# Performance work log

Hardware: AMD Instinct MI355X
Metric: run time of the kernel (lower is better)

## Reference

```python
import jax, jax.numpy as jnp
import numpy as np
from jax import lax

SEQ, B, I, H, O = 512, 64, 512, 1024, 512


def _linear_params(key, out_f, in_f):
    kw, kb = jax.random.split(key)
    bound = 1.0 / np.sqrt(in_f)
    W = jax.random.uniform(kw, (out_f, in_f), jnp.float32, -bound, bound)
    b = jax.random.uniform(kb, (out_f,), jnp.float32, -bound, bound)
    return W, b


def setup_inputs() -> dict:
    key = jax.random.key(0)
    ks = jax.random.split(key, 8)
    x = jax.random.normal(ks[0], (SEQ, B, I), jnp.float32)
    Wxz, bxz = _linear_params(ks[1], H, I)
    Whz, bhz = _linear_params(ks[2], H, H)
    Wxr, bxr = _linear_params(ks[3], H, I)
    Whr, bhr = _linear_params(ks[4], H, H)
    Wxh, bxh = _linear_params(ks[5], H, I)
    Whh, bhh = _linear_params(ks[6], H, H)
    Why, bhy = _linear_params(ks[7], O, H)
    return {"x": x, "Wxz": Wxz, "bxz": bxz, "Whz": Whz, "bhz": bhz,
            "Wxr": Wxr, "bxr": bxr, "Whr": Whr, "bhr": bhr,
            "Wxh": Wxh, "bxh": bxh, "Whh": Whh, "bhh": bhh,
            "Why": Why, "bhy": bhy}


def reference(x, Wxz, bxz, Whz, bhz, Wxr, bxr, Whr, bhr, Wxh, bxh, Whh, bhh, Why, bhy):
    # Precompute all input-side projections in batched GEMMs: [S,B,H]
    xz = jnp.einsum('sbi,hi->sbh', x, Wxz) + bxz
    xr = jnp.einsum('sbi,hi->sbh', x, Wxr) + bxr
    xh = jnp.einsum('sbi,hi->sbh', x, Wxh) + bxh

    def step(h, inp):
        xz_t, xr_t, xh_t = inp
        z = jax.nn.sigmoid(xz_t + h @ Whz.T + bhz)
        r = jax.nn.sigmoid(xr_t + h @ Whr.T + bhr)
        h_cand = jnp.tanh(xh_t + r * (h @ Whh.T + bhh))
        h_new = (1.0 - z) * h + z * h_cand
        return h_new, h_new

    h0 = jnp.zeros((x.shape[1], Whz.shape[0]), x.dtype)
    _, hs = lax.scan(step, h0, (xz, xr, xh))  # hs: [S,B,H]
    out = jnp.einsum('sbh,oh->sbo', hs, Why) + bhy  # [S,B,O]
    return out
```

## Files before the change

### kernel.cpp

```cpp
#include <hip/hip_runtime.h>
#include <hip/hip_bf16.h>

#define SEQL 512
#define BATCH 64
#define INF 512
#define HID 1024
#define OUTF 512
#define SB (SEQL*BATCH)
#define BH (BATCH*HID)

typedef __attribute__((ext_vector_type(8))) __bf16 bf16x8;
typedef __attribute__((ext_vector_type(4))) float f32x4;

__device__ inline bf16x8 ld_bf8(const void* p) { return *reinterpret_cast<const bf16x8*>(p); }
__device__ inline unsigned short f2bf(float f) { __bf16 b = (__bf16)f; return __builtin_bit_cast(unsigned short, b); }

__device__ inline void st_u64c(void* p, unsigned long long v) {
    __hip_atomic_store((unsigned long long*)p, v, __ATOMIC_RELAXED, __HIP_MEMORY_SCOPE_AGENT);
}

__global__ void cvt_f32_bf16(const float* __restrict__ src, unsigned short* __restrict__ dst, int n) {
    int i = (blockIdx.x * blockDim.x + threadIdx.x) * 4;
    if (i < n) {
        float4 v = *reinterpret_cast<const float4*>(src + i);
        ushort4 o = make_ushort4(f2bf(v.x), f2bf(v.y), f2bf(v.z), f2bf(v.w));
        *reinterpret_cast<ushort4*>(dst + i) = o;
    }
}

__global__ void make_bias2(const float* bxz, const float* bhz, const float* bxr,
                           const float* bhr, float* bias2) {
    int i = blockIdx.x * blockDim.x + threadIdx.x;
    if (i < HID) bias2[i] = bxz[i] + bhz[i];
    else if (i < 2*HID) bias2[i] = bxr[i-HID] + bhr[i-HID];
}

__global__ void fail_sentinel(float* o) { o[0] = 1e9f; }

__global__ __launch_bounds__(256, 2) void gemm_nt_f32(
        const unsigned short* __restrict__ A, int lda,
        const unsigned short* __restrict__ Bw, int ldb,
        const float* __restrict__ bias,
        float* __restrict__ Cf, int N, int K) {
    __shared__ __align__(16) char lds[32768];
    const int tid = threadIdx.x;
    const int ntn = N >> 7;
    const int bm = blockIdx.x / ntn, bn = blockIdx.x % ntn;
    const int rowbase = bm << 7, colbase = bn << 7;
    const int wave = tid >> 6, lane = tid & 63, lo = lane & 15, hi = lane >> 4;
    const int vm = wave >> 1, vn = wave & 1;

    auto stage = [&](int abase, int k0) {
        #pragma unroll
        for (int i = 0; i < 2; i++) {
            int linear = i * 256 + tid;
            int r = linear >> 2, s = linear & 3;
            int c = (s - (r >> 1)) & 3;
            const unsigned short* ga = A + (size_t)(rowbase + r) * lda + k0 + c * 8;
            const unsigned short* gb = Bw + (size_t)(colbase + r) * ldb + k0 + c * 8;
            __builtin_amdgcn_global_load_lds(
                (const __attribute__((address_space(1))) unsigned int*)ga,
                (__attribute__((address_space(3))) unsigned int*)(lds + abase + linear * 16), 16, 0, 0);
            __builtin_amdgcn_global_load_lds(
                (const __attribute__((address_space(1))) unsigned int*)gb,
                (__attribute__((address_space(3))) unsigned int*)(lds + 16384 + abase + linear * 16), 16, 0, 0);
        }
    };

    f32x4 acc[4][4] = {};
    const int nk = K >> 5;
    stage(0, 0);
    for (int kt = 0; kt < nk; kt++) {
        __syncthreads();
        if (kt + 1 < nk) stage(((kt + 1) & 1) * 8192, (kt + 1) << 5);
        const char* cA = lds + (kt & 1) * 8192;
        const char* cB = lds + 16384 + (kt & 1) * 8192;
        bf16x8 af[4], bfr[4];
        #pragma unroll
        for (int m = 0; m < 4; m++) {
            int r = vm * 64 + m * 16 + lo;
            af[m] = ld_bf8(cA + r * 64 + 16 * ((hi + (r >> 1)) & 3));
        }
        #pragma unroll
        for (int n = 0; n < 4; n++) {
            int r = vn * 64 + n * 16 + lo;
            bfr[n] = ld_bf8(cB + r * 64 + 16 * ((hi + (r >> 1)) & 3));
        }
        #pragma unroll
        for (int m = 0; m < 4; m++)
            #pragma unroll
            for (int n = 0; n < 4; n++)
                acc[m][n] = __builtin_amdgcn_mfma_f32_16x16x32_bf16(af[m], bfr[n], acc[m][n], 0, 0, 0);
        __syncthreads();
    }

    #pragma unroll
    for (int n = 0; n < 4; n++) {
        int col = colbase + vn * 64 + n * 16 + lo;
        float bv = bias[col];
        #pragma unroll
        for (int m = 0; m < 4; m++)
            #pragma unroll
            for (int r = 0; r < 4; r++) {
                int row = rowbase + vm * 64 + m * 16 + hi * 4 + r;
                Cf[(size_t)row * N + col] = acc[m][n][r] + bv;
            }
    }
}

__global__ __launch_bounds__(192, 1) void gru_scan(
        const unsigned short* __restrict__ Whc,
        const unsigned short* __restrict__ Wxc,
        const unsigned short* __restrict__ xbf,
        unsigned short* __restrict__ hs,
        const float* __restrict__ bias2,
        const float* __restrict__ bxh,
        const float* __restrict__ bhh,
        unsigned int* flags) {
    __shared__ __align__(16) char lds[134656];
    const int tid = threadIdx.x;
    const int wid = blockIdx.x;
    const int rb = wid >> 6;
    const int cb = wid & 63;
    const int g = tid / 64;
    const int lane = tid & 63, lo = lane & 15, hi = lane >> 4;
    const int col = cb * 16 + lo;
    char* whl = lds + g * 32768;
    char* hstage = lds + 98304;
    f32x4* Px = (f32x4*)(lds + 131072);
    unsigned short* T = (unsigned short*)(lds + 134144);

    {
        const unsigned short* ph = Whc + ((size_t)g * HID + col) * HID + hi * 8;
        #pragma unroll
        for (int kb = 0; kb < 32; kb++)
            __builtin_amdgcn_global_load_lds(
                (const __attribute__((address_space(1))) unsigned int*)(ph + kb * 32),
                (__attribute__((address_space(3))) unsigned int*)(whl + kb * 1024 + lane * 16), 16, 0, 0);
    }
    __syncthreads();
    asm volatile("buffer_inv sc0 sc1" ::: "memory");

    const float bzv  = bias2[col];
    const float brv  = bias2[HID + col];
    const float bxhv = bxh[col];
    const float bhhv = bhh[col];
    float hst[4] = {0.f, 0.f, 0.f, 0.f};
    const unsigned short* wxp = Wxc + ((size_t)g * HID + col) * INF + hi * 8;
    const unsigned int* flA = flags + rb * 64 + (lane & 31);
    const unsigned int* flB = flags + rb * 64 + 32 + (lane & 31);

    f32x4 ax = {0,0,0,0};
    {
        const unsigned short* xp = xbf + ((size_t)(rb * 16 + lo)) * INF + hi * 8;
        #pragma unroll
        for (int kb = 0; kb < 16; kb++)
            ax = __builtin_amdgcn_mfma_f32_16x16x32_bf16(ld_bf8(xp + kb * 32), ld_bf8(wxp + kb * 32), ax, 0, 0, 0);
    }

    for (int t = 0; t < SEQL; t++) {
        if (t > 0) {
            const unsigned short* hsrc = hs + (size_t)t * BH + (size_t)(rb * 16) * HID;
            #pragma unroll
            for (int it = 0; it < 6; it++) {
                int v = it * 192 + tid;
                if (v < 1024)
                    __builtin_amdgcn_global_load_lds(
                        (const __attribute__((address_space(1))) unsigned int*)(hsrc + (size_t)(v & 15) * HID + (v >> 4) * 8),
                        (__attribute__((address_space(3))) unsigned int*)(hstage + v * 16), 16, 0, 0 );
            }
            {
                unsigned int tgt = (unsigned int)t;
                while (!__all(__hip_atomic_load(flB, __ATOMIC_RELAXED, __HIP_MEMORY_SCOPE_AGENT) >= tgt))
                    __builtin_amdgcn_s_sleep(1);
            }
            #pragma unroll
            for (int it = 0; it < 6; it++) {
                int v = 1024 + it * 192 + tid;
                if (v < 2048)
                    __builtin_amdgcn_global_load_lds(
                        (const __attribute__((address_space(1))) unsigned int*)(hsrc + (size_t)(v & 15) * HID + (v >> 4) * 8),
                        (__attribute__((address_space(3))) unsigned int*)(hstage + v * 16), 16, 0, 0);
            }
        }
        __syncthreads();

        f32x4 ah = {0,0,0,0};
        if (t > 0) {
            #pragma unroll
            for (int kb = 0; kb < 32; kb++) {
                bf16x8 w = ld_bf8(whl + kb * 1024 + lane * 16);
                bf16x8 a = ld_bf8(hstage + kb * 1024 + lane * 16);
                ah = __builtin_amdgcn_mfma_f32_16x16x32_bf16(a, w, ah, 0, 0, 0);
            }
        }

        if (g == 1) {
            f32x4 v;
            #pragma unroll
            for (int r = 0; r < 4; r++) v[r] = ah[r] + ax[r] + brv;
            Px[0 * 64 + lane] = v;
        } else if (g == 2) {
            f32x4 v, w;
            #pragma unroll
            for (int r = 0; r < 4; r++) { v[r] = ah[r] + bhhv; w[r] = ax[r] + bxhv; }
            Px[1 * 64 + lane] = v;
            Px[2 * 64 + lane] = w;
        }
        __syncthreads();

        if (g == 0) {
            unsigned short* hdst = hs + (size_t)(t + 1) * BH;
            f32x4 pr = Px[0 * 64 + lane];
            f32x4 ph_ = Px[1 * 64 + lane];
            f32x4 px_ = Px[2 * 64 + lane];
            #pragma unroll
            for (int r = 0; r < 4; r++) {
                float z  = 1.f / (1.f + __expf(-(ah[r] + ax[r] + bzv)));
                float rr = 1.f / (1.f + __expf(-pr[r]));
                float hc = tanhf(px_[r] + rr * ph_[r]);
                hst[r] = (1.f - z) * hst[r] + z * hc;
                T[(hi * 4 + r) * 16 + lo] = f2bf(hst[r]);
            }
            asm volatile("s_waitcnt lgkmcnt(0)" ::: "memory");
            int row = lane >> 2, q = lane & 3;
            unsigned long long val = *(const unsigned long long*)(T + row * 16 + q * 4);
            st_u64c(hdst + (size_t)(rb * 16 + row) * HID + cb * 16 + q * 4, val);
            asm volatile("s_waitcnt vmcnt(0)" ::: "memory");
        }
        if (tid == 0)
            __hip_atomic_store(flags + rb * 64 + cb, (unsigned int)(t + 1),
                               __ATOMIC_RELAXED, __HIP_MEMORY_SCOPE_AGENT);

        f32x4 nax = {0,0,0,0};
        if (t + 1 < SEQL) {
            const unsigned short* xp = xbf + ((size_t)(t + 1) * BATCH + rb * 16 + lo) * INF + hi * 8;
            #pragma unroll
            for (int kb = 0; kb < 16; kb++)
                nax = __builtin_amdgcn_mfma_f32_16x16x32_bf16(ld_bf8(xp + kb * 32), ld_bf8(wxp + kb * 32), nax, 0, 0, 0);
            unsigned int tgt = (unsigned int)(t + 1);
            while (!__all(__hip_atomic_load(flA, __ATOMIC_RELAXED, __HIP_MEMORY_SCOPE_AGENT) >= tgt))
                __builtin_amdgcn_s_sleep(1);
        }
        ax = nax;
    }
}

extern "C" void kernel_launch(void* const* d_in, const int* in_sizes, int n_in,
                              void* d_out, int out_size, void* d_ws, size_t ws_size,
                              hipStream_t stream) {
    const float* x   = (const float*)d_in[0];
    const float* Wxz = (const float*)d_in[1];
    const float* bxz = (const float*)d_in[2];
    const float* Whz = (const float*)d_in[3];
    const float* bhz = (const float*)d_in[4];
    const float* Wxr = (const float*)d_in[5];
    const float* bxr = (const float*)d_in[6];
    const float* Whr = (const float*)d_in[7];
    const float* bhr = (const float*)d_in[8];
    const float* Wxh = (const float*)d_in[9];
    const float* bxh = (const float*)d_in[10];
    const float* Whh = (const float*)d_in[11];
    const float* bhh = (const float*)d_in[12];
    const float* Why = (const float*)d_in[13];
    const float* bhy = (const float*)d_in[14];

    char* ws = (char*)d_ws;
    size_t off = 0;
    auto alloc = [&](size_t bytes) { char* p = ws + off; off += (bytes + 255) & ~(size_t)255; return p; };
    unsigned short* Whc   = (unsigned short*)alloc((size_t)3 * HID * HID * 2);
    unsigned short* Wxc   = (unsigned short*)alloc((size_t)3 * HID * INF * 2);
    unsigned short* Whyb  = (unsigned short*)alloc((size_t)OUTF * HID * 2);
    float*          bias2 = (float*)alloc((size_t)2 * HID * 4);
    unsigned short* hsbuf = (unsigned short*)alloc((size_t)(SEQL + 1) * BATCH * HID * 2);
    unsigned int*   flags = (unsigned int*)alloc(1024);
    unsigned short* x_bf  = (unsigned short*)d_out;

    if (off > ws_size) {
        fail_sentinel<<<dim3(1), dim3(1), 0, stream>>>((float*)d_out);
        return;
    }

    auto cvt = [&](const float* s, unsigned short* d, size_t n) {
        cvt_f32_bf16<<<dim3((unsigned)((n / 4 + 255) / 256)), dim3(256), 0, stream>>>(s, d, (int)n);
    };
    cvt(x, x_bf, (size_t)SB * INF);
    cvt(Whz, Whc, (size_t)HID * HID);
    cvt(Whr, Whc + (size_t)HID * HID, (size_t)HID * HID);
    cvt(Whh, Whc + (size_t)2 * HID * HID, (size_t)HID * HID);
    cvt(Wxz, Wxc, (size_t)HID * INF);
    cvt(Wxr, Wxc + (size_t)HID * INF, (size_t)HID * INF);
    cvt(Wxh, Wxc + (size_t)2 * HID * INF, (size_t)HID * INF);
    cvt(Why, Whyb, (size_t)OUTF * HID);
    make_bias2<<<dim3(8), dim3(256), 0, stream>>>(bxz, bhz, bxr, bhr, bias2);
    (void)hipMemsetAsync(flags, 0, 1024, stream);

    gru_scan<<<dim3(256), dim3(192), 0, stream>>>(Whc, Wxc, x_bf, hsbuf, bias2, bxh, bhh, flags);

    gemm_nt_f32<<<dim3((SB / 128) * (OUTF / 128)), dim3(256), 0, stream>>>(
        hsbuf + (size_t)BATCH * HID, HID, Whyb, HID, bhy, (float*)d_out, OUTF, HID);
}
```

Before: 2.921 ms.

## Store hidden states in MFMA-fragment-major layout for contiguous scan loads

The hidden-state history buffer changes from row-major [t][batch][hid] to a fragment-major layout in which each 16-row batch block's k-chunks of 16 rows by 8 elements are contiguous. The per-step global-to-LDS staging in the scan then reads fully contiguous 16-byte chunks instead of strided rows, and each workgroup's write of its 16x16 tile becomes a single contiguous 512-byte store. The output GEMM's A-operand addressing is rewritten to index this layout. Compiler memory barriers are added after the flag spin-waits.

```diff
diff --git a/kernel.cpp b/kernel.cpp
--- a/kernel.cpp
+++ b/kernel.cpp
@@ -38,7 +38,7 @@
 __global__ void fail_sentinel(float* o) { o[0] = 1e9f; }
 
 __global__ __launch_bounds__(256, 2) void gemm_nt_f32(
-        const unsigned short* __restrict__ A, int lda,
+        const unsigned short* __restrict__ A,
         const unsigned short* __restrict__ Bw, int ldb,
         const float* __restrict__ bias,
         float* __restrict__ Cf, int N, int K) {
@@ -56,7 +56,9 @@
             int linear = i * 256 + tid;
             int r = linear >> 2, s = linear & 3;
             int c = (s - (r >> 1)) & 3;
-            const unsigned short* ga = A + (size_t)(rowbase + r) * lda + k0 + c * 8;
+            int R = rowbase + r;
+            const unsigned short* ga = A + ((size_t)(R >> 6) * 65536 + (size_t)((R >> 4) & 3) * 16384
+                                     + (size_t)((((k0 + c * 8) >> 3) * 16) + (R & 15)) * 8);
             const unsigned short* gb = Bw + (size_t)(colbase + r) * ldb + k0 + c * 8;
             __builtin_amdgcn_global_load_lds(
                 (const __attribute__((address_space(1))) unsigned int*)ga,
@@ -112,7 +114,7 @@
         const unsigned short* __restrict__ Whc,
         const unsigned short* __restrict__ Wxc,
         const unsigned short* __restrict__ xbf,
-        unsigned short* __restrict__ hs,
+        unsigned short* __restrict__ hsFM,
         const float* __restrict__ bias2,
         const float* __restrict__ bxh,
         const float* __restrict__ bhh,
@@ -160,26 +162,27 @@
 
     for (int t = 0; t < SEQL; t++) {
         if (t > 0) {
-            const unsigned short* hsrc = hs + (size_t)t * BH + (size_t)(rb * 16) * HID;
+            const unsigned short* hf = hsFM + (size_t)t * 65536 + rb * 16384;
             #pragma unroll
             for (int it = 0; it < 6; it++) {
                 int v = it * 192 + tid;
                 if (v < 1024)
                     __builtin_amdgcn_global_load_lds(
-                        (const __attribute__((address_space(1))) unsigned int*)(hsrc + (size_t)(v & 15) * HID + (v >> 4) * 8),
-                        (__attribute__((address_space(3))) unsigned int*)(hstage + v * 16), 16, 0, 0 );
+                        (const __attribute__((address_space(1))) unsigned int*)(hf + v * 8),
+                        (__attribute__((address_space(3))) unsigned int*)(hstage + v * 16), 16, 0, 0);
             }
             {
                 unsigned int tgt = (unsigned int)t;
                 while (!__all(__hip_atomic_load(flB, __ATOMIC_RELAXED, __HIP_MEMORY_SCOPE_AGENT) >= tgt))
                     __builtin_amdgcn_s_sleep(1);
+                asm volatile("" ::: "memory");
             }
             #pragma unroll
             for (int it = 0; it < 6; it++) {
                 int v = 1024 + it * 192 + tid;
                 if (v < 2048)
                     __builtin_amdgcn_global_load_lds(
-                        (const __attribute__((address_space(1))) unsigned int*)(hsrc + (size_t)(v & 15) * HID + (v >> 4) * 8),
+                        (const __attribute__((address_space(1))) unsigned int*)(hf + v * 8),
                         (__attribute__((address_space(3))) unsigned int*)(hstage + v * 16), 16, 0, 0);
             }
         }
@@ -210,7 +213,6 @@
         __syncthreads();
 
         if (g == 0) {
-            unsigned short* hdst = hs + (size_t)(t + 1) * BH;
             f32x4 pr = Px[0 * 64 + lane];
             f32x4 ph_ = Px[1 * 64 + lane];
             f32x4 px_ = Px[2 * 64 + lane];
@@ -223,9 +225,9 @@
                 T[(hi * 4 + r) * 16 + lo] = f2bf(hst[r]);
             }
             asm volatile("s_waitcnt lgkmcnt(0)" ::: "memory");
-            int row = lane >> 2, q = lane & 3;
-            unsigned long long val = *(const unsigned long long*)(T + row * 16 + q * 4);
-            st_u64c(hdst + (size_t)(rb * 16 + row) * HID + cb * 16 + q * 4, val);
+            unsigned short* fmdst = hsFM + (size_t)(t + 1) * 65536 + rb * 16384 + cb * 256;
+            st_u64c(fmdst + lane * 4,
+                    *(const unsigned long long*)(T + ((lane >> 1) & 15) * 16 + (lane >> 5) * 8 + (lane & 1) * 4));
             asm volatile("s_waitcnt vmcnt(0)" ::: "memory");
         }
         if (tid == 0)
@@ -241,6 +243,7 @@
             unsigned int tgt = (unsigned int)(t + 1);
             while (!__all(__hip_atomic_load(flA, __ATOMIC_RELAXED, __HIP_MEMORY_SCOPE_AGENT) >= tgt))
                 __builtin_amdgcn_s_sleep(1);
+            asm volatile("" ::: "memory");
         }
         ax = nax;
     }
@@ -272,7 +275,7 @@
     unsigned short* Wxc   = (unsigned short*)alloc((size_t)3 * HID * INF * 2);
     unsigned short* Whyb  = (unsigned short*)alloc((size_t)OUTF * HID * 2);
     float*          bias2 = (float*)alloc((size_t)2 * HID * 4);
-    unsigned short* hsbuf = (unsigned short*)alloc((size_t)(SEQL + 1) * BATCH * HID * 2);
+    unsigned short* hsFM  = (unsigned short*)alloc((size_t)(SEQL + 1) * 65536 * 2);
     unsigned int*   flags = (unsigned int*)alloc(1024);
     unsigned short* x_bf  = (unsigned short*)d_out;
 
@@ -295,8 +298,8 @@
     make_bias2<<<dim3(8), dim3(256), 0, stream>>>(bxz, bhz, bxr, bhr, bias2);
     (void)hipMemsetAsync(flags, 0, 1024, stream);
 
-    gru_scan<<<dim3(256), dim3(192), 0, stream>>>(Whc, Wxc, x_bf, hsbuf, bias2, bxh, bhh, flags);
+    gru_scan<<<dim3(256), dim3(192), 0, stream>>>(Whc, Wxc, x_bf, hsFM, bias2, bxh, bhh, flags);
 
     gemm_nt_f32<<<dim3((SB / 128) * (OUTF / 128)), dim3(256), 0, stream>>>(
-        hsbuf + (size_t)BATCH * HID, HID, Whyb, HID, bhy, (float*)d_out, OUTF, HID);
-}
+        hsFM + 65536, Whyb, HID, bhy, (float*)d_out, OUTF, HID);
+}
```

New measurement: 2.857 ms. 2.2% less time.
